# Kernel tuning notes

Hardware: AMD Instinct MI355X
Metric: run time of the kernel (lower is better)

The kernel has to match this reference:

```python
import jax, jax.numpy as jnp
import numpy as np

N, M, E, F, OUT = 20000, 2048, 320000, 512, 2
HID = F // 2
NEG_ATT = 0.2   # leaky_relu slope inside HypergraphConv attention
NEG = 0.01      # default F.leaky_relu / nn.LeakyReLU slope
EPS = 1e-5      # GraphNorm eps


def setup_inputs() -> dict:
    key = jax.random.key(0)
    ks = jax.random.split(key, 12)
    nrm = lambda k, shape, s=0.05: (jax.random.normal(k, shape, jnp.float32) * s)
    row = jax.random.randint(ks[1], (E,), 0, N)
    col = jax.random.randint(ks[2], (E,), 0, M)
    return dict(
        x=nrm(ks[0], (N, F), 1.0),
        edge_index=jnp.stack([row, col]),                 # [2, E] int32
        edge_attr=nrm(ks[3], (M, F), 1.0),
        W1=nrm(ks[4], (F, F)), att1=nrm(ks[5], (2 * F,)), b1=jnp.zeros((F,), jnp.float32),
        W2=nrm(ks[6], (F, F)), att2=nrm(ks[7], (2 * F,)), b2=jnp.zeros((F,), jnp.float32),
        gn1_w=jnp.ones((F,), jnp.float32), gn1_b=jnp.zeros((F,), jnp.float32), gn1_ms=jnp.ones((F,), jnp.float32),
        gn2_w=jnp.ones((F,), jnp.float32), gn2_b=jnp.zeros((F,), jnp.float32), gn2_ms=jnp.ones((F,), jnp.float32),
        fc1_W=nrm(ks[8], (F, HID)), fc1_b=jnp.zeros((HID,), jnp.float32),
        fc2_W=nrm(ks[9], (F, HID)), fc2_b=jnp.zeros((HID,), jnp.float32),
        cls_W=nrm(ks[10], (HID, OUT)), cls_b=jnp.zeros((OUT,), jnp.float32),
    )


def _segsum(v, idx, n):
    return jax.ops.segment_sum(v, idx, num_segments=n)


def hypergraph_conv(x, edge_attr, row, col, W, att, bias):
    """PyG HypergraphConv, heads=1, use_attention=True, attention_mode='node'."""
    xl = x @ W                          # [N, F] node features after lin
    el = edge_attr @ W                  # [M, F] hyperedge features after lin
    # attention logits per incidence: (cat[x_i, e_j] * att).sum(-1)
    pre = xl[row] @ att[:F] + el[col] @ att[F:]           # [E]
    alpha = jax.nn.leaky_relu(pre, NEG_ATT)
    # softmax grouped by hyperedge (col)
    amax = jax.ops.segment_max(alpha, col, num_segments=M)
    amax = jnp.where(jnp.isfinite(amax), amax, 0.0)
    ex = jnp.exp(alpha - amax[col])
    denom = _segsum(ex, col, M)
    alpha = ex / jnp.maximum(denom, 1e-16)[col]           # [E]
    # degree normalizations (hyperedge_weight = 1)
    ones = jnp.ones((row.shape[0],), xl.dtype)
    deg_n = _segsum(ones, row, N)
    Dinv = jnp.where(deg_n > 0, 1.0 / deg_n, 0.0)         # [N]
    deg_e = _segsum(ones, col, M)
    Binv = jnp.where(deg_e > 0, 1.0 / deg_e, 0.0)         # [M]
    # propagate 1: nodes -> hyperedges
    edge_feat = _segsum((alpha * Binv[col])[:, None] * xl[row], col, M)   # [M, F]
    # propagate 2: hyperedges -> nodes
    out = _segsum((alpha * Dinv[row])[:, None] * edge_feat[col], row, N)  # [N, F]
    return out + bias


def graph_norm(x, w, b, ms):
    # single graph (batch=None): normalize over all nodes
    mean = x.mean(axis=0)
    out = x - ms * mean
    var = (out * out).mean(axis=0)
    return out / jnp.sqrt(var + EPS) * w + b


def reference(x, edge_index, edge_attr,
              W1, att1, b1, W2, att2, b2,
              gn1_w, gn1_b, gn1_ms, gn2_w, gn2_b, gn2_ms,
              fc1_W, fc1_b, fc2_W, fc2_b, cls_W, cls_b):
    row, col = edge_index[0], edge_index[1]
    h = hypergraph_conv(x, edge_attr, row, col, W1, att1, b1)
    h = jax.nn.leaky_relu(graph_norm(h, gn1_w, gn1_b, gn1_ms), NEG)
    out = jax.nn.leaky_relu(h @ fc1_W + fc1_b, NEG)
    h = hypergraph_conv(h, edge_attr, row, col, W2, att2, b2)
    h = jax.nn.leaky_relu(graph_norm(h, gn2_w, gn2_b, gn2_ms), NEG)
    out = out + jax.nn.leaky_relu(h @ fc2_W + fc2_b, NEG)
    logits = out @ cls_W + cls_b
    return logits
```

## Files before the change

### kernel.cpp

```cpp
#include <hip/hip_runtime.h>
#include <math.h>

#define FDIM 512
#define HIDDIM 256
#define HB 128
#define SCH 1024
#define LDSK 32

typedef __bf16 bf16x8 __attribute__((ext_vector_type(8)));
typedef float floatx4 __attribute__((ext_vector_type(4)));

__device__ __forceinline__ float lrelu(float x, float s) { return x >= 0.0f ? x : s * x; }

__device__ __forceinline__ float bf2f(unsigned int u) {
  union { float f; unsigned int i; } v; v.i = u << 16; return v.f;
}
__device__ __forceinline__ unsigned short f2bf(float f) {
  union { float f; unsigned int u; } v; v.f = f;
  unsigned int x = v.u;
  return (unsigned short)((x + 0x7fffu + ((x >> 16) & 1u)) >> 16);
}

__device__ __forceinline__ void async_copy16(const unsigned short* g, unsigned short* l) {
  __builtin_amdgcn_global_load_lds((const __attribute__((address_space(1))) unsigned int*)g,
                                   (__attribute__((address_space(3))) unsigned int*)l, 16, 0, 0);
}

__device__ __forceinline__ float waveReduceSum(float v) {
#pragma unroll
  for (int o = 32; o; o >>= 1) v += __shfl_down(v, o, 64);
  return v;
}

__device__ __forceinline__ float blockReduceSum256(float v) {
  __shared__ float sm[4];
  int lane = threadIdx.x & 63, w = threadIdx.x >> 6;
  v = waveReduceSum(v);
  __syncthreads();
  if (lane == 0) sm[w] = v;
  __syncthreads();
  return sm[0] + sm[1] + sm[2] + sm[3];
}

__device__ __forceinline__ float blockReduceMax256(float v) {
  __shared__ float sm[4];
  int lane = threadIdx.x & 63, w = threadIdx.x >> 6;
#pragma unroll
  for (int o = 32; o; o >>= 1) v = fmaxf(v, __shfl_down(v, o, 64));
  __syncthreads();
  if (lane == 0) sm[w] = v;
  __syncthreads();
  return fmaxf(fmaxf(sm[0], sm[1]), fmaxf(sm[2], sm[3]));
}

__global__ __launch_bounds__(256) void k_hist2(const int* __restrict__ row, const int* __restrict__ col,
                                               int* __restrict__ cnt_r, int* __restrict__ cnt_c,
                                               int E, int nchunk) {
  __shared__ int h[2048];
  int b = blockIdx.x, t = threadIdx.x;
  for (int i = t; i < 2048; i += 256) h[i] = 0;
  __syncthreads();
  int s = b * nchunk, e = min(E, s + nchunk);
  for (int j = s + t; j < e; j += 256) {
    atomicAdd(&h[col[j]], 1);
    atomicAdd(&cnt_r[row[j]], 1);
  }
  __syncthreads();
  for (int i = t; i < 2048; i += 256) {
    int v = h[i];
    if (v) atomicAdd(&cnt_c[i], v);
  }
}

__global__ __launch_bounds__(256) void k_scan_part(const int* __restrict__ cnt, int* __restrict__ off,
                                                   int* __restrict__ btot, int n) {
  int b = blockIdx.x, t = threadIdx.x;
  int base = b * SCH + t * 4;
  int v[4];
#pragma unroll
  for (int i = 0; i < 4; ++i) v[i] = (base + i < n) ? cnt[base + i] : 0;
  int s = v[0] + v[1] + v[2] + v[3];
  int lane = t & 63, w = t >> 6;
  int x = s;
#pragma unroll
  for (int o = 1; o < 64; o <<= 1) {
    int y = __shfl_up(x, o, 64);
    if (lane >= o) x += y;
  }
  __shared__ int ws[4];
  if (lane == 63) ws[w] = x;
  __syncthreads();
  int wpre = 0;
  for (int i = 0; i < w; ++i) wpre += ws[i];
  int run = wpre + x - s;
#pragma unroll
  for (int i = 0; i < 4; ++i) {
    if (base + i < n) off[base + i] = run;
    run += v[i];
  }
  if (t == 255) btot[b] = wpre + x;
}

__global__ __launch_bounds__(256) void k_scan_mid(int* __restrict__ btot, int nb) {
  int t = threadIdx.x;
  int v = (t < nb) ? btot[t] : 0;
  int lane = t & 63, w = t >> 6;
  int x = v;
#pragma unroll
  for (int o = 1; o < 64; o <<= 1) {
    int y = __shfl_up(x, o, 64);
    if (lane >= o) x += y;
  }
  __shared__ int ws[4];
  if (lane == 63) ws[w] = x;
  __syncthreads();
  int wpre = 0;
  for (int i = 0; i < w; ++i) wpre += ws[i];
  if (t < nb) btot[t] = wpre + x - v;
  if (t == 255) btot[nb] = wpre + x;
}

__global__ __launch_bounds__(256) void k_scan_add(int* __restrict__ off, const int* __restrict__ btot,
                                                  int n, int nb) {
  int b = blockIdx.x, t = threadIdx.x;
  int base = b * SCH + t * 4;
  int add = btot[b];
#pragma unroll
  for (int i = 0; i < 4; ++i)
    if (base + i < n) off[base + i] += add;
  if (b == 0 && t == 0) off[n] = btot[nb];
}

__global__ __launch_bounds__(256) void k_scan2048(const int* __restrict__ cnt, int* __restrict__ off,
                                                  int* __restrict__ gcur) {
  int t = threadIdx.x;
  int base = t * 8;
  int v[8];
#pragma unroll
  for (int i = 0; i < 8; ++i) v[i] = cnt[base + i];
  int s = 0;
#pragma unroll
  for (int i = 0; i < 8; ++i) s += v[i];
  int lane = t & 63, w = t >> 6;
  int x = s;
#pragma unroll
  for (int o = 1; o < 64; o <<= 1) {
    int y = __shfl_up(x, o, 64);
    if (lane >= o) x += y;
  }
  __shared__ int ws[4];
  if (lane == 63) ws[w] = x;
  __syncthreads();
  int wpre = 0;
  for (int i = 0; i < w; ++i) wpre += ws[i];
  int run = wpre + x - s;
#pragma unroll
  for (int i = 0; i < 8; ++i) {
    off[base + i] = run;
    gcur[base + i] = run;
    run += v[i];
  }
  if (t == 255) off[2048] = wpre + x;
}

__global__ __launch_bounds__(256) void k_fill3(const int* __restrict__ row, const int* __restrict__ col,
                                               int* __restrict__ gcur, const int* __restrict__ off_r,
                                               int* __restrict__ cur_r, int* __restrict__ csr_c,
                                               int* __restrict__ rj, int* __restrict__ cj,
                                               int* __restrict__ pos_r, int E, int nchunk) {
  __shared__ int h[2048];
  __shared__ int lbase[2048];
  int b = blockIdx.x, t = threadIdx.x;
  for (int i = t; i < 2048; i += 256) h[i] = 0;
  __syncthreads();
  int s = b * nchunk, e = min(E, s + nchunk);
  for (int j = s + t; j < e; j += 256) atomicAdd(&h[col[j]], 1);
  __syncthreads();
  for (int i = t; i < 2048; i += 256) {
    int c = h[i];
    lbase[i] = c ? atomicAdd(&gcur[i], c) : 0;
    h[i] = 0;
  }
  __syncthreads();
  for (int j = s + t; j < e; j += 256) {
    int r = row[j], c = col[j];
    int slot_c = lbase[c] + atomicAdd(&h[c], 1);
    csr_c[slot_c] = j;
    rj[slot_c] = r;
    int slot_r = off_r[r] + atomicAdd(&cur_r[r], 1);
    cj[slot_r] = c;
    pos_r[j] = slot_r;
  }
}

__global__ __launch_bounds__(256) void k_sortseg(int* __restrict__ rj, int* __restrict__ csr_c,
                                                 const int* __restrict__ off_c) {
  int m = blockIdx.x;
  int s = off_c[m], e = off_c[m + 1];
  int n = e - s;
  if (n > 512) return;
  __shared__ int key[512];
  __shared__ int val[512];
  int t = threadIdx.x;
  for (int i = t; i < 512; i += 256) {
    if (i < n) { key[i] = rj[s + i]; val[i] = csr_c[s + i]; }
    else { key[i] = 0x7fffffff; val[i] = 0; }
  }
  __syncthreads();
  for (int k = 2; k <= 512; k <<= 1) {
    for (int j = k >> 1; j > 0; j >>= 1) {
#pragma unroll
      for (int p = 0; p < 2; ++p) {
        int i = t + p * 256;
        int ixj = i ^ j;
        if (ixj > i) {
          bool up = ((i & k) == 0);
          int a = key[i], b = key[ixj];
          if ((a > b) == up) {
            key[i] = b; key[ixj] = a;
            int va = val[i]; val[i] = val[ixj]; val[ixj] = va;
          }
        }
      }
      __syncthreads();
    }
  }
  for (int i = t; i < n; i += 256) {
    rj[s + i] = key[i];
    csr_c[s + i] = val[i];
  }
}

__global__ __launch_bounds__(256) void k_hi(const float* __restrict__ A, unsigned short* __restrict__ hi, int n4) {
  int i = blockIdx.x * 256 + threadIdx.x;
  if (i < n4) {
    float4 v = ((const float4*)A)[i];
    ushort4 h;
    h.x = f2bf(v.x); h.y = f2bf(v.y); h.z = f2bf(v.z); h.w = f2bf(v.w);
    ((ushort4*)hi)[i] = h;
  }
}

__global__ __launch_bounds__(256) void k_prep_w_hi(const float* __restrict__ W, unsigned short* __restrict__ th,
                                                   int K, int Nc) {
  int n = blockIdx.x * 16 + (threadIdx.x & 15);
  int k = blockIdx.y * 16 + (threadIdx.x >> 4);
  th[(size_t)n * K + k] = f2bf(W[(size_t)k * Nc + n]);
}

__global__ __launch_bounds__(256) void k_prep_w(const float* __restrict__ W, unsigned short* __restrict__ th,
                                                unsigned short* __restrict__ tl, int K, int Nc) {
  int n = blockIdx.x * 16 + (threadIdx.x & 15);
  int k = blockIdx.y * 16 + (threadIdx.x >> 4);
  float v = W[(size_t)k * Nc + n];
  unsigned short h = f2bf(v);
  unsigned short l = f2bf(v - bf2f(h));
  th[(size_t)n * K + k] = h;
  tl[(size_t)n * K + k] = l;
}

__global__ __launch_bounds__(256) void k_wv2(const float* __restrict__ W1, const float* __restrict__ a1,
                                             const float* __restrict__ W2, const float* __restrict__ a2,
                                             float* __restrict__ wv1, float* __restrict__ wv2) {
  int lane = threadIdx.x & 63, w = threadIdx.x >> 6;
  int k = blockIdx.x * 4 + w;
  const float* W = blockIdx.y ? W2 : W1;
  const float* a = blockIdx.y ? a2 : a1;
  float* wv = blockIdx.y ? wv2 : wv1;
  float s = 0.f;
  for (int f = lane; f < FDIM; f += 64) s = fmaf(W[(size_t)k * FDIM + f], a[f], s);
  s = waveReduceSum(s);
  if (lane == 0) wv[k] = s;
}

__global__ __launch_bounds__(256) void k_ea2(const float* __restrict__ X, const float* __restrict__ wv1,
                                             const float* __restrict__ wv2, float* __restrict__ ea1,
                                             float* __restrict__ ea2, int Mr) {
  int lane = threadIdx.x & 63, w = threadIdx.x >> 6;
  int m = blockIdx.x * 4 + w;
  if (m < Mr) {
    float s1 = 0.f, s2 = 0.f;
    for (int f = lane; f < FDIM; f += 64) {
      float v = X[(size_t)m * FDIM + f];
      s1 = fmaf(v, wv1[f], s1);
      s2 = fmaf(v, wv2[f], s2);
    }
    s1 = waveReduceSum(s1);
    s2 = waveReduceSum(s2);
    if (lane == 0) { ea1[m] = s1; ea2[m] = s2; }
  }
}

__global__ __launch_bounds__(256, 1) void gemm_conv(const unsigned short* __restrict__ Ah,
                                                    const unsigned short* __restrict__ Bth,
                                                    unsigned short* __restrict__ Cb,
                                                    const float* __restrict__ att, float* __restrict__ xa,
                                                    int Mr, int K, int Nc) {
  __shared__ unsigned short lds[2 * 128 * LDSK];
  int tid = threadIdx.x, lane = tid & 63, w = tid >> 6;
  int wr = w >> 1, wc = w & 1;
  int rowB = blockIdx.y * 128, colB = blockIdx.x * 128;

  const unsigned short* src = (w < 2) ? Ah : Bth;
  int baseRow = ((w < 2) ? rowB : colB) + 64 * (w & 1);
  int maxRow = (w < 2) ? (Mr - 1) : (Nc - 1);
  int slr = lane >> 2, slc = lane & 3;
  unsigned short* dstBase = &lds[((w >> 1) * 128 + (w & 1) * 64) * LDSK];

  size_t gro[4];
#pragma unroll
  for (int seg = 0; seg < 4; ++seg) {
    int rg = baseRow + seg * 16 + slr;
    if (rg > maxRow) rg = maxRow;
    gro[seg] = (size_t)rg * K + slc * 8;
  }

  floatx4 zero4 = {0.f, 0.f, 0.f, 0.f};
  floatx4 acc[4][4];
#pragma unroll
  for (int i = 0; i < 4; ++i)
#pragma unroll
    for (int j = 0; j < 4; ++j) acc[i][j] = zero4;

  int fr = lane & 15, fq = lane >> 4;
  int offA = (wr * 64 + fr) * LDSK + fq * 8;
  int offB = 128 * LDSK + (wc * 64 + fr) * LDSK + fq * 8;

  for (int k0 = 0; k0 < K; k0 += 32) {
#pragma unroll
    for (int seg = 0; seg < 4; ++seg) async_copy16(src + gro[seg] + k0, dstBase + seg * 16 * LDSK);
    __syncthreads();
    bf16x8 a[4], b[4];
#pragma unroll
    for (int t = 0; t < 4; ++t) {
      a[t] = *(const bf16x8*)(&lds[offA + t * 16 * LDSK]);
      b[t] = *(const bf16x8*)(&lds[offB + t * 16 * LDSK]);
    }
#pragma unroll
    for (int ti = 0; ti < 4; ++ti)
#pragma unroll
      for (int tj = 0; tj < 4; ++tj)
        acc[ti][tj] = __builtin_amdgcn_mfma_f32_16x16x32_bf16(a[ti], b[tj], acc[ti][tj], 0, 0, 0);
    __syncthreads();
  }

  int colL = colB + wc * 64 + fr;
  int rowL = rowB + wr * 64 + fq * 4;
  float attv[4];
#pragma unroll
  for (int tj = 0; tj < 4; ++tj) attv[tj] = att[colL + tj * 16];
#pragma unroll
  for (int ti = 0; ti < 4; ++ti) {
#pragma unroll
    for (int r = 0; r < 4; ++r) {
      int rr = rowL + ti * 16 + r;
      if (rr < Mr) {
        float dot = 0.f;
#pragma unroll
        for (int tj = 0; tj < 4; ++tj) {
          float v = acc[ti][tj][r];
          Cb[(size_t)rr * Nc + colL + tj * 16] = f2bf(v);
          dot = fmaf(v, attv[tj], dot);
        }
#pragma unroll
        for (int o = 1; o < 16; o <<= 1) dot += __shfl_xor(dot, o, 64);
        if ((lane & 15) == 0) atomicAdd(&xa[rr], dot);
      }
    }
  }
}

template <int EPI>
__global__ __launch_bounds__(256, 1) void gemm_fc(const unsigned short* __restrict__ Ahi,
                                                  const unsigned short* __restrict__ Bthi,
                                                  const unsigned short* __restrict__ Btlo,
                                                  float* __restrict__ Cf, const float* __restrict__ bias,
                                                  int Mr, int K, int Nc) {
  __shared__ unsigned short lds[3 * 128 * LDSK];
  int tid = threadIdx.x, lane = tid & 63, w = tid >> 6;
  int wr = w >> 1, wc = w & 1;
  int rowB = blockIdx.y * 128, colB = blockIdx.x * 128;

  const unsigned short* src;
  int baseRow, maxRow, nseg;
  unsigned short* dstBase;
  if (w < 2) { src = Ahi; baseRow = rowB + 64 * w; maxRow = Mr - 1; nseg = 4; dstBase = &lds[w * 64 * LDSK]; }
  else if (w == 2) { src = Bthi; baseRow = colB; maxRow = Nc - 1; nseg = 8; dstBase = &lds[128 * LDSK]; }
  else { src = Btlo; baseRow = colB; maxRow = Nc - 1; nseg = 8; dstBase = &lds[2 * 128 * LDSK]; }

  int slr = lane >> 2, slc = lane & 3;
  size_t gro[8];
  for (int seg = 0; seg < nseg; ++seg) {
    int rg = baseRow + seg * 16 + slr;
    if (rg > maxRow) rg = maxRow;
    gro[seg] = (size_t)rg * K + slc * 8;
  }

  floatx4 zero4 = {0.f, 0.f, 0.f, 0.f};
  floatx4 acc[4][4];
#pragma unroll
  for (int i = 0; i < 4; ++i)
#pragma unroll
    for (int j = 0; j < 4; ++j) acc[i][j] = zero4;

  int fr = lane & 15, fq = lane >> 4;
  int offA = (wr * 64 + fr) * LDSK + fq * 8;
  int offBh = 128 * LDSK + (wc * 64 + fr) * LDSK + fq * 8;

  for (int k0 = 0; k0 < K; k0 += 32) {
    for (int seg = 0; seg < nseg; ++seg) async_copy16(src + gro[seg] + k0, dstBase + seg * 16 * LDSK);
    __syncthreads();
    bf16x8 a[4], bh[4], bl[4];
#pragma unroll
    for (int t = 0; t < 4; ++t) {
      a[t] = *(const bf16x8*)(&lds[offA + t * 16 * LDSK]);
      bh[t] = *(const bf16x8*)(&lds[offBh + t * 16 * LDSK]);
      bl[t] = *(const bf16x8*)(&lds[128 * LDSK + offBh + t * 16 * LDSK]);
    }
#pragma unroll
    for (int ti = 0; ti < 4; ++ti)
#pragma unroll
      for (int tj = 0; tj < 4; ++tj) {
        acc[ti][tj] = __builtin_amdgcn_mfma_f32_16x16x32_bf16(a[ti], bh[tj], acc[ti][tj], 0, 0, 0);
        acc[ti][tj] = __builtin_amdgcn_mfma_f32_16x16x32_bf16(a[ti], bl[tj], acc[ti][tj], 0, 0, 0);
      }
    __syncthreads();
  }

  int colL = colB + wc * 64 + fr;
  int rowL = rowB + wr * 64 + fq * 4;
#pragma unroll
  for (int tj = 0; tj < 4; ++tj) {
    int c = colL + tj * 16;
    float bb = bias[c];
#pragma unroll
    for (int ti = 0; ti < 4; ++ti) {
#pragma unroll
      for (int r = 0; r < 4; ++r) {
        int rr = rowL + ti * 16 + r;
        if (rr < Mr) {
          float v = lrelu(acc[ti][tj][r] + bb, 0.01f);
          if (EPI == 1) Cf[(size_t)rr * Nc + c] = v;
          else Cf[(size_t)rr * Nc + c] += v;
        }
      }
    }
  }
}

__global__ __launch_bounds__(256) void k_attn(const float* __restrict__ xa, const float* __restrict__ ea,
                                              const int* __restrict__ rj, const int* __restrict__ csr_c,
                                              const int* __restrict__ pos_r, const int* __restrict__ off_c,
                                              float* __restrict__ aj, float* __restrict__ arj) {
  int m = blockIdx.x;
  int s = off_c[m], e_ = off_c[m + 1];
  float eam = ea[m];
  int t = threadIdx.x;
  float mx = -3.402823466e38f;
  for (int j = s + t; j < e_; j += 256) {
    float a = lrelu(xa[rj[j]] + eam, 0.2f);
    aj[j] = a;
    mx = fmaxf(mx, a);
  }
  mx = blockReduceMax256(mx);
  float sum = 0.f;
  for (int j = s + t; j < e_; j += 256) sum += expf(aj[j] - mx);
  sum = blockReduceSum256(sum);
  float inv = 1.0f / fmaxf(sum, 1e-16f);
  for (int j = s + t; j < e_; j += 256) {
    float a = expf(aj[j] - mx) * inv;
    aj[j] = a;
    arj[pos_r[csr_c[j]]] = a;
  }
}

__global__ __launch_bounds__(256) void k_prop_col(const unsigned short* __restrict__ xl,
                                                  const float* __restrict__ aj, const int* __restrict__ rj,
                                                  const int* __restrict__ off_c, unsigned short* __restrict__ ef) {
  int m = blockIdx.x;
  int s = off_c[m], e_ = off_c[m + 1];
  int cnt = e_ - s;
  __shared__ int sidx[512];
  __shared__ float swgt[512];
  __shared__ float pf[4][512];
  int t = threadIdx.x, lane = t & 63, w = t >> 6;
  float acc[8] = {0, 0, 0, 0, 0, 0, 0, 0};
  for (int base = 0; base < cnt; base += 512) {
    int n = min(512, cnt - base);
    for (int j = t; j < n; j += 256) {
      sidx[j] = rj[s + base + j];
      swgt[j] = aj[s + base + j];
    }
    __syncthreads();
    int j = w;
    for (; j + 16 <= n; j += 16) {
      int r0 = sidx[j], r1 = sidx[j + 4], r2 = sidx[j + 8], r3 = sidx[j + 12];
      float w0 = swgt[j], w1 = swgt[j + 4], w2 = swgt[j + 8], w3 = swgt[j + 12];
      bf16x8 v0 = *(const bf16x8*)(xl + (size_t)r0 * FDIM + lane * 8);
      bf16x8 v1 = *(const bf16x8*)(xl + (size_t)r1 * FDIM + lane * 8);
      bf16x8 v2 = *(const bf16x8*)(xl + (size_t)r2 * FDIM + lane * 8);
      bf16x8 v3 = *(const bf16x8*)(xl + (size_t)r3 * FDIM + lane * 8);
#pragma unroll
      for (int i = 0; i < 8; ++i) acc[i] = fmaf(w0, (float)v0[i], acc[i]);
#pragma unroll
      for (int i = 0; i < 8; ++i) acc[i] = fmaf(w1, (float)v1[i], acc[i]);
#pragma unroll
      for (int i = 0; i < 8; ++i) acc[i] = fmaf(w2, (float)v2[i], acc[i]);
#pragma unroll
      for (int i = 0; i < 8; ++i) acc[i] = fmaf(w3, (float)v3[i], acc[i]);
    }
    for (; j < n; j += 4) {
      int r = sidx[j];
      float wt = swgt[j];
      bf16x8 v = *(const bf16x8*)(xl + (size_t)r * FDIM + lane * 8);
#pragma unroll
      for (int i = 0; i < 8; ++i) acc[i] = fmaf(wt, (float)v[i], acc[i]);
    }
    __syncthreads();
  }
  float binv = cnt > 0 ? 1.0f / (float)cnt : 0.0f;
#pragma unroll
  for (int i = 0; i < 8; i += 2) *(float2*)&pf[w][lane * 8 + i] = make_float2(acc[i] * binv, acc[i + 1] * binv);
  __syncthreads();
  float2 r0 = ((const float2*)pf[0])[t], r1 = ((const float2*)pf[1])[t];
  float2 r2 = ((const float2*)pf[2])[t], r3 = ((const float2*)pf[3])[t];
  float a0 = r0.x + r1.x + r2.x + r3.x;
  float a1 = r0.y + r1.y + r2.y + r3.y;
  unsigned int o = (unsigned int)f2bf(a0) | ((unsigned int)f2bf(a1) << 16);
  ((unsigned int*)(ef + (size_t)m * FDIM))[t] = o;
}

__global__ __launch_bounds__(256) void k_prop_row(const unsigned short* __restrict__ ef,
                                                  const float* __restrict__ arj, const int* __restrict__ cj,
                                                  const int* __restrict__ off_r, const float* __restrict__ bias,
                                                  unsigned short* __restrict__ hb) {
  int nB = blockIdx.x;
  int s = off_r[nB], e_ = off_r[nB + 1];
  int cnt = e_ - s;
  __shared__ int sidx[512];
  __shared__ float swgt[512];
  __shared__ float pf[4][512];
  int t = threadIdx.x, lane = t & 63, w = t >> 6;
  float acc[8] = {0, 0, 0, 0, 0, 0, 0, 0};
  for (int base = 0; base < cnt; base += 512) {
    int n = min(512, cnt - base);
    for (int j = t; j < n; j += 256) {
      sidx[j] = cj[s + base + j];
      swgt[j] = arj[s + base + j];
    }
    __syncthreads();
    int j = w;
    for (; j + 8 <= n; j += 8) {
      int r0 = sidx[j], r1 = sidx[j + 4];
      float w0 = swgt[j], w1 = swgt[j + 4];
      bf16x8 v0 = *(const bf16x8*)(ef + (size_t)r0 * FDIM + lane * 8);
      bf16x8 v1 = *(const bf16x8*)(ef + (size_t)r1 * FDIM + lane * 8);
#pragma unroll
      for (int i = 0; i < 8; ++i) acc[i] = fmaf(w0, (float)v0[i], acc[i]);
#pragma unroll
      for (int i = 0; i < 8; ++i) acc[i] = fmaf(w1, (float)v1[i], acc[i]);
    }
    for (; j < n; j += 4) {
      int r = sidx[j];
      float wt = swgt[j];
      bf16x8 v = *(const bf16x8*)(ef + (size_t)r * FDIM + lane * 8);
#pragma unroll
      for (int i = 0; i < 8; ++i) acc[i] = fmaf(wt, (float)v[i], acc[i]);
    }
    __syncthreads();
  }
  float dinv = cnt > 0 ? 1.0f / (float)cnt : 0.0f;
#pragma unroll
  for (int i = 0; i < 8; i += 2) *(float2*)&pf[w][lane * 8 + i] = make_float2(acc[i] * dinv, acc[i + 1] * dinv);
  __syncthreads();
  float2 r0 = ((const float2*)pf[0])[t], r1 = ((const float2*)pf[1])[t];
  float2 r2 = ((const float2*)pf[2])[t], r3 = ((const float2*)pf[3])[t];
  float a0 = r0.x + r1.x + r2.x + r3.x + bias[2 * t];
  float a1 = r0.y + r1.y + r2.y + r3.y + bias[2 * t + 1];
  unsigned int o = (unsigned int)f2bf(a0) | ((unsigned int)f2bf(a1) << 16);
  ((unsigned int*)(hb + (size_t)nB * FDIM))[t] = o;
}

__global__ __launch_bounds__(256) void k_stats(const unsigned short* __restrict__ hb, float* __restrict__ gsum,
                                               float* __restrict__ gsq, int N) {
  int t = threadIdx.x;
  float s0 = 0, q0 = 0, s1 = 0, q1 = 0;
  for (int r = blockIdx.x; r < N; r += gridDim.x) {
    unsigned int u = ((const unsigned int*)(hb + (size_t)r * FDIM))[t];
    float v0 = bf2f(u & 0xffffu), v1 = bf2f(u >> 16);
    s0 += v0; q0 = fmaf(v0, v0, q0);
    s1 += v1; q1 = fmaf(v1, v1, q1);
  }
  atomicAdd(&gsum[2 * t], s0);
  atomicAdd(&gsq[2 * t], q0);
  atomicAdd(&gsum[2 * t + 1], s1);
  atomicAdd(&gsq[2 * t + 1], q1);
}

__global__ __launch_bounds__(512) void k_nparam(const float* __restrict__ gsum, const float* __restrict__ gsq,
                                                const float* __restrict__ ms, const float* __restrict__ w,
                                                float* __restrict__ msm, float* __restrict__ scl, float invn) {
  int f = threadIdx.x;
  float mean = gsum[f] * invn;
  float ex2 = gsq[f] * invn;
  float m = ms[f];
  float var = ex2 - (2.0f * m - m * m) * mean * mean;
  scl[f] = w[f] / sqrtf(var + 1e-5f);
  msm[f] = m * mean;
}

__global__ __launch_bounds__(256) void k_napply(const unsigned short* __restrict__ hb,
                                                const float* __restrict__ msm, const float* __restrict__ scl,
                                                const float* __restrict__ b, unsigned short* __restrict__ hi,
                                                int total2) {
  int i = blockIdx.x * 256 + threadIdx.x;
  if (i < total2) {
    int f2 = i & 255;
    unsigned int u = ((const unsigned int*)hb)[i];
    float v0 = bf2f(u & 0xffffu), v1 = bf2f(u >> 16);
    int f0 = 2 * f2, f1 = 2 * f2 + 1;
    v0 = lrelu((v0 - msm[f0]) * scl[f0] + b[f0], 0.01f);
    v1 = lrelu((v1 - msm[f1]) * scl[f1] + b[f1], 0.01f);
    ((unsigned int*)hi)[i] = (unsigned int)f2bf(v0) | ((unsigned int)f2bf(v1) << 16);
  }
}

__global__ __launch_bounds__(256) void k_cls(const float* __restrict__ out1, const float* __restrict__ W,
                                             const float* __restrict__ b, float* __restrict__ logits, int N) {
  __shared__ float Ws[512];
  int t = threadIdx.x;
  Ws[t] = W[t];
  Ws[256 + t] = W[256 + t];
  __syncthreads();
  int lane = t & 63, w = t >> 6;
  int r = blockIdx.x * 4 + w;
  if (r < N) {
    float a0 = 0.f, a1 = 0.f;
    for (int k = lane; k < 256; k += 64) {
      float v = out1[(size_t)r * 256 + k];
      a0 = fmaf(v, Ws[2 * k], a0);
      a1 = fmaf(v, Ws[2 * k + 1], a1);
    }
#pragma unroll
    for (int o = 32; o; o >>= 1) {
      a0 += __shfl_down(a0, o, 64);
      a1 += __shfl_down(a1, o, 64);
    }
    if (lane == 0) {
      logits[(size_t)r * 2] = a0 + b[0];
      logits[(size_t)r * 2 + 1] = a1 + b[1];
    }
  }
}

extern "C" void kernel_launch(void* const* d_in, const int* in_sizes, int n_in,
                              void* d_out, int out_size, void* d_ws, size_t ws_size,
                              hipStream_t stream) {
  const float* x      = (const float*)d_in[0];
  const int*   eidx   = (const int*)d_in[1];
  const float* eattr  = (const float*)d_in[2];
  const float* W1     = (const float*)d_in[3];
  const float* att1   = (const float*)d_in[4];
  const float* b1     = (const float*)d_in[5];
  const float* W2     = (const float*)d_in[6];
  const float* att2   = (const float*)d_in[7];
  const float* b2     = (const float*)d_in[8];
  const float* gn1_w  = (const float*)d_in[9];
  const float* gn1_b  = (const float*)d_in[10];
  const float* gn1_ms = (const float*)d_in[11];
  const float* gn2_w  = (const float*)d_in[12];
  const float* gn2_b  = (const float*)d_in[13];
  const float* gn2_ms = (const float*)d_in[14];
  const float* fc1_W  = (const float*)d_in[15];
  const float* fc1_b  = (const float*)d_in[16];
  const float* fc2_W  = (const float*)d_in[17];
  const float* fc2_b  = (const float*)d_in[18];
  const float* cls_W  = (const float*)d_in[19];
  const float* cls_b  = (const float*)d_in[20];
  float* logits = (float*)d_out;

  const int N = in_sizes[0] / FDIM;
  const int E = in_sizes[1] / 2;
  const int M = in_sizes[2] / FDIM;
  const int* row = eidx;
  const int* col = eidx + E;
  const size_t NS = (size_t)N * FDIM;
  const size_t MS = (size_t)M * FDIM;

  char* base = (char*)d_ws;
  auto alloc = [&](size_t bytes) { char* r = base; base += (bytes + 255) & ~(size_t)255; return r; };

  unsigned short* xhi = (unsigned short*)alloc(NS * 2);
  unsigned short* xl  = (unsigned short*)alloc(NS * 2);
  unsigned short* hb  = (unsigned short*)alloc(NS * 2);
  unsigned short* ef  = (unsigned short*)alloc(MS * 2);
  float* out1 = (float*)alloc((size_t)N * HIDDIM * 4);
  unsigned short* w1th = (unsigned short*)alloc(FDIM * FDIM * 2);
  unsigned short* w2th = (unsigned short*)alloc(FDIM * FDIM * 2);
  unsigned short* f1th = (unsigned short*)alloc(FDIM * HIDDIM * 2);
  unsigned short* f1tl = (unsigned short*)alloc(FDIM * HIDDIM * 2);
  unsigned short* f2th = (unsigned short*)alloc(FDIM * HIDDIM * 2);
  unsigned short* f2tl = (unsigned short*)alloc(FDIM * HIDDIM * 2);
  float* wv1 = (float*)alloc(FDIM * 4);
  float* wv2 = (float*)alloc(FDIM * 4);
  float* xa = (float*)alloc((size_t)N * 4);
  float* ea1 = (float*)alloc((size_t)M * 4);
  float* ea2 = (float*)alloc((size_t)M * 4);
  float* aj  = (float*)alloc((size_t)E * 4);
  float* arj = (float*)alloc((size_t)E * 4);
  float* gsum = (float*)alloc(FDIM * 4);
  float* gsq  = (float*)alloc(FDIM * 4);
  float* msm  = (float*)alloc(FDIM * 4);
  float* scl  = (float*)alloc(FDIM * 4);
  int* cnt_r = (int*)alloc((size_t)(2 * N + M) * 4);
  int* cur_r = cnt_r + N;
  int* cnt_c = cur_r + N;
  int* off_r = (int*)alloc((size_t)(N + 1) * 4);
  int* off_c = (int*)alloc((size_t)(M + 1) * 4);
  int* gcur  = (int*)alloc((size_t)M * 4);
  int* csr_c = (int*)alloc((size_t)E * 4);
  int* rj    = (int*)alloc((size_t)E * 4);
  int* cj    = (int*)alloc((size_t)E * 4);
  int* pos_r = (int*)alloc((size_t)E * 4);
  int* btot  = (int*)alloc(512 * 4);

  hipMemsetAsync(cnt_r, 0, sizeof(int) * (size_t)(2 * N + M), stream);

  int nchunk = (E + HB - 1) / HB;
  int nbR = (N + SCH - 1) / SCH;
  k_hist2<<<HB, 256, 0, stream>>>(row, col, cnt_r, cnt_c, E, nchunk);
  k_scan_part<<<nbR, 256, 0, stream>>>(cnt_r, off_r, btot, N);
  k_scan_mid<<<1, 256, 0, stream>>>(btot, nbR);
  k_scan_add<<<nbR, 256, 0, stream>>>(off_r, btot, N, nbR);
  k_scan2048<<<1, 256, 0, stream>>>(cnt_c, off_c, gcur);
  k_fill3<<<HB, 256, 0, stream>>>(row, col, gcur, off_r, cur_r, csr_c, rj, cj, pos_r, E, nchunk);
  k_sortseg<<<M, 256, 0, stream>>>(rj, csr_c, off_c);

  k_hi<<<(int)((NS / 4 + 255) / 256), 256, 0, stream>>>(x, xhi, (int)(NS / 4));
  k_prep_w_hi<<<dim3(FDIM / 16, FDIM / 16), 256, 0, stream>>>(W1, w1th, FDIM, FDIM);
  k_prep_w_hi<<<dim3(FDIM / 16, FDIM / 16), 256, 0, stream>>>(W2, w2th, FDIM, FDIM);
  k_prep_w<<<dim3(HIDDIM / 16, FDIM / 16), 256, 0, stream>>>(fc1_W, f1th, f1tl, FDIM, HIDDIM);
  k_prep_w<<<dim3(HIDDIM / 16, FDIM / 16), 256, 0, stream>>>(fc2_W, f2th, f2tl, FDIM, HIDDIM);
  k_wv2<<<dim3(FDIM / 4, 2), 256, 0, stream>>>(W1, att1 + FDIM, W2, att2 + FDIM, wv1, wv2);
  k_ea2<<<(M + 3) / 4, 256, 0, stream>>>(eattr, wv1, wv2, ea1, ea2, M);

  int gN128 = (N + 127) / 128;
  int napply_grid = (int)((NS / 2 + 255) / 256);

  hipMemsetAsync(xa, 0, (size_t)N * 4, stream);
  gemm_conv<<<dim3(FDIM / 128, gN128), 256, 0, stream>>>(xhi, w1th, xl, att1, xa, N, FDIM, FDIM);
  k_attn<<<M, 256, 0, stream>>>(xa, ea1, rj, csr_c, pos_r, off_c, aj, arj);
  k_prop_col<<<M, 256, 0, stream>>>(xl, aj, rj, off_c, ef);
  k_prop_row<<<N, 256, 0, stream>>>(ef, arj, cj, off_r, b1, hb);
  hipMemsetAsync(gsum, 0, sizeof(float) * 2 * FDIM, stream);
  k_stats<<<256, 256, 0, stream>>>(hb, gsum, gsq, N);
  k_nparam<<<1, 512, 0, stream>>>(gsum, gsq, gn1_ms, gn1_w, msm, scl, 1.0f / (float)N);
  k_napply<<<napply_grid, 256, 0, stream>>>(hb, msm, scl, gn1_b, xhi, (int)(NS / 2));
  gemm_fc<1><<<dim3(HIDDIM / 128, gN128), 256, 0, stream>>>(xhi, f1th, f1tl, out1, fc1_b, N, FDIM, HIDDIM);

  hipMemsetAsync(xa, 0, (size_t)N * 4, stream);
  gemm_conv<<<dim3(FDIM / 128, gN128), 256, 0, stream>>>(xhi, w2th, xl, att2, xa, N, FDIM, FDIM);
  k_attn<<<M, 256, 0, stream>>>(xa, ea2, rj, csr_c, pos_r, off_c, aj, arj);
  k_prop_col<<<M, 256, 0, stream>>>(xl, aj, rj, off_c, ef);
  k_prop_row<<<N, 256, 0, stream>>>(ef, arj, cj, off_r, b2, hb);
  hipMemsetAsync(gsum, 0, sizeof(float) * 2 * FDIM, stream);
  k_stats<<<256, 256, 0, stream>>>(hb, gsum, gsq, N);
  k_nparam<<<1, 512, 0, stream>>>(gsum, gsq, gn2_ms, gn2_w, msm, scl, 1.0f / (float)N);
  k_napply<<<napply_grid, 256, 0, stream>>>(hb, msm, scl, gn2_b, xhi, (int)(NS / 2));
  gemm_fc<2><<<dim3(HIDDIM / 128, gN128), 256, 0, stream>>>(xhi, f2th, f2tl, out1, fc2_b, N, FDIM, HIDDIM);

  k_cls<<<(N + 3) / 4, 256, 0, stream>>>(out1, cls_W, cls_b, logits, N);
}
```

Measured before the change: 601.8 us.

## Fuse attention softmax into column propagation and cut small launches and memsets

Attention softmax is folded into the column-propagation kernel, which recomputes logits from xa instead of storing and rereading a per-incidence buffer. The per-segment bitonic sort is dropped, and the column scan is merged into the mid-scan kernel. Weight preparation is batched into two launches, the norm-parameter kernel is folded into napply, and all zeroing becomes one memset. The cost is recomputing exp/lrelu three times per incidence; dropping the sort changes the order of segment sums, which may change rounding and access locality.

```diff
diff --git a/kernel.cpp b/kernel.cpp
--- a/kernel.cpp
+++ b/kernel.cpp
@@ -101,23 +101,52 @@
   if (t == 255) btot[b] = wpre + x;
 }
 
-__global__ __launch_bounds__(256) void k_scan_mid(int* __restrict__ btot, int nb) {
-  int t = threadIdx.x;
-  int v = (t < nb) ? btot[t] : 0;
-  int lane = t & 63, w = t >> 6;
-  int x = v;
-#pragma unroll
-  for (int o = 1; o < 64; o <<= 1) {
-    int y = __shfl_up(x, o, 64);
-    if (lane >= o) x += y;
-  }
+__global__ __launch_bounds__(256) void k_scan_midcol(int* __restrict__ btot, int nb,
+                                                     const int* __restrict__ cnt_c, int* __restrict__ off_c,
+                                                     int* __restrict__ gcur) {
+  int t = threadIdx.x, lane = t & 63, w = t >> 6;
   __shared__ int ws[4];
-  if (lane == 63) ws[w] = x;
-  __syncthreads();
-  int wpre = 0;
-  for (int i = 0; i < w; ++i) wpre += ws[i];
-  if (t < nb) btot[t] = wpre + x - v;
-  if (t == 255) btot[nb] = wpre + x;
+  if (blockIdx.x == 0) {
+    int v = (t < nb) ? btot[t] : 0;
+    int x = v;
+#pragma unroll
+    for (int o = 1; o < 64; o <<= 1) {
+      int y = __shfl_up(x, o, 64);
+      if (lane >= o) x += y;
+    }
+    if (lane == 63) ws[w] = x;
+    __syncthreads();
+    int wpre = 0;
+    for (int i = 0; i < w; ++i) wpre += ws[i];
+    if (t < nb) btot[t] = wpre + x - v;
+    if (t == 255) btot[nb] = wpre + x;
+  } else {
+    int base = t * 8;
+    int v[8];
+#pragma unroll
+    for (int i = 0; i < 8; ++i) v[i] = cnt_c[base + i];
+    int s = 0;
+#pragma unroll
+    for (int i = 0; i < 8; ++i) s += v[i];
+    int x = s;
+#pragma unroll
+    for (int o = 1; o < 64; o <<= 1) {
+      int y = __shfl_up(x, o, 64);
+      if (lane >= o) x += y;
+    }
+    if (lane == 63) ws[w] = x;
+    __syncthreads();
+    int wpre = 0;
+    for (int i = 0; i < w; ++i) wpre += ws[i];
+    int run = wpre + x - s;
+#pragma unroll
+    for (int i = 0; i < 8; ++i) {
+      off_c[base + i] = run;
+      gcur[base + i] = run;
+      run += v[i];
+    }
+    if (t == 255) off_c[2048] = wpre + x;
+  }
 }
 
 __global__ __launch_bounds__(256) void k_scan_add(int* __restrict__ off, const int* __restrict__ btot,
@@ -129,38 +158,6 @@
   for (int i = 0; i < 4; ++i)
     if (base + i < n) off[base + i] += add;
   if (b == 0 && t == 0) off[n] = btot[nb];
-}
-
-__global__ __launch_bounds__(256) void k_scan2048(const int* __restrict__ cnt, int* __restrict__ off,
-                                                  int* __restrict__ gcur) {
-  int t = threadIdx.x;
-  int base = t * 8;
-  int v[8];
-#pragma unroll
-  for (int i = 0; i < 8; ++i) v[i] = cnt[base + i];
-  int s = 0;
-#pragma unroll
-  for (int i = 0; i < 8; ++i) s += v[i];
-  int lane = t & 63, w = t >> 6;
-  int x = s;
-#pragma unroll
-  for (int o = 1; o < 64; o <<= 1) {
-    int y = __shfl_up(x, o, 64);
-    if (lane >= o) x += y;
-  }
-  __shared__ int ws[4];
-  if (lane == 63) ws[w] = x;
-  __syncthreads();
-  int wpre = 0;
-  for (int i = 0; i < w; ++i) wpre += ws[i];
-  int run = wpre + x - s;
-#pragma unroll
-  for (int i = 0; i < 8; ++i) {
-    off[base + i] = run;
-    gcur[base + i] = run;
-    run += v[i];
-  }
-  if (t == 255) off[2048] = wpre + x;
 }
 
 __global__ __launch_bounds__(256) void k_fill3(const int* __restrict__ row, const int* __restrict__ col,
@@ -193,44 +190,6 @@
   }
 }
 
-__global__ __launch_bounds__(256) void k_sortseg(int* __restrict__ rj, int* __restrict__ csr_c,
-                                                 const int* __restrict__ off_c) {
-  int m = blockIdx.x;
-  int s = off_c[m], e = off_c[m + 1];
-  int n = e - s;
-  if (n > 512) return;
-  __shared__ int key[512];
-  __shared__ int val[512];
-  int t = threadIdx.x;
-  for (int i = t; i < 512; i += 256) {
-    if (i < n) { key[i] = rj[s + i]; val[i] = csr_c[s + i]; }
-    else { key[i] = 0x7fffffff; val[i] = 0; }
-  }
-  __syncthreads();
-  for (int k = 2; k <= 512; k <<= 1) {
-    for (int j = k >> 1; j > 0; j >>= 1) {
-#pragma unroll
-      for (int p = 0; p < 2; ++p) {
-        int i = t + p * 256;
-        int ixj = i ^ j;
-        if (ixj > i) {
-          bool up = ((i & k) == 0);
-          int a = key[i], b = key[ixj];
-          if ((a > b) == up) {
-            key[i] = b; key[ixj] = a;
-            int va = val[i]; val[i] = val[ixj]; val[ixj] = va;
-          }
-        }
-      }
-      __syncthreads();
-    }
-  }
-  for (int i = t; i < n; i += 256) {
-    rj[s + i] = key[i];
-    csr_c[s + i] = val[i];
-  }
-}
-
 __global__ __launch_bounds__(256) void k_hi(const float* __restrict__ A, unsigned short* __restrict__ hi, int n4) {
   int i = blockIdx.x * 256 + threadIdx.x;
   if (i < n4) {
@@ -241,15 +200,23 @@
   }
 }
 
-__global__ __launch_bounds__(256) void k_prep_w_hi(const float* __restrict__ W, unsigned short* __restrict__ th,
-                                                   int K, int Nc) {
+__global__ __launch_bounds__(256) void k_prep_w_hi2(const float* __restrict__ W1, unsigned short* __restrict__ t1,
+                                                    const float* __restrict__ W2, unsigned short* __restrict__ t2,
+                                                    int K, int Nc) {
+  const float* W = blockIdx.z ? W2 : W1;
+  unsigned short* th = blockIdx.z ? t2 : t1;
   int n = blockIdx.x * 16 + (threadIdx.x & 15);
   int k = blockIdx.y * 16 + (threadIdx.x >> 4);
   th[(size_t)n * K + k] = f2bf(W[(size_t)k * Nc + n]);
 }
 
-__global__ __launch_bounds__(256) void k_prep_w(const float* __restrict__ W, unsigned short* __restrict__ th,
-                                                unsigned short* __restrict__ tl, int K, int Nc) {
+__global__ __launch_bounds__(256) void k_prep_w2(const float* __restrict__ Wa, unsigned short* __restrict__ tha,
+                                                 unsigned short* __restrict__ tla, const float* __restrict__ Wb,
+                                                 unsigned short* __restrict__ thb, unsigned short* __restrict__ tlb,
+                                                 int K, int Nc) {
+  const float* W = blockIdx.z ? Wb : Wa;
+  unsigned short* th = blockIdx.z ? thb : tha;
+  unsigned short* tl = blockIdx.z ? tlb : tla;
   int n = blockIdx.x * 16 + (threadIdx.x & 15);
   int k = blockIdx.y * 16 + (threadIdx.x >> 4);
   float v = W[(size_t)k * Nc + n];
@@ -448,48 +415,38 @@
   }
 }
 
-__global__ __launch_bounds__(256) void k_attn(const float* __restrict__ xa, const float* __restrict__ ea,
-                                              const int* __restrict__ rj, const int* __restrict__ csr_c,
-                                              const int* __restrict__ pos_r, const int* __restrict__ off_c,
-                                              float* __restrict__ aj, float* __restrict__ arj) {
-  int m = blockIdx.x;
-  int s = off_c[m], e_ = off_c[m + 1];
-  float eam = ea[m];
-  int t = threadIdx.x;
-  float mx = -3.402823466e38f;
-  for (int j = s + t; j < e_; j += 256) {
-    float a = lrelu(xa[rj[j]] + eam, 0.2f);
-    aj[j] = a;
-    mx = fmaxf(mx, a);
-  }
-  mx = blockReduceMax256(mx);
-  float sum = 0.f;
-  for (int j = s + t; j < e_; j += 256) sum += expf(aj[j] - mx);
-  sum = blockReduceSum256(sum);
-  float inv = 1.0f / fmaxf(sum, 1e-16f);
-  for (int j = s + t; j < e_; j += 256) {
-    float a = expf(aj[j] - mx) * inv;
-    aj[j] = a;
-    arj[pos_r[csr_c[j]]] = a;
-  }
-}
-
-__global__ __launch_bounds__(256) void k_prop_col(const unsigned short* __restrict__ xl,
-                                                  const float* __restrict__ aj, const int* __restrict__ rj,
-                                                  const int* __restrict__ off_c, unsigned short* __restrict__ ef) {
+__global__ __launch_bounds__(256) void k_prop_col_f(const unsigned short* __restrict__ xl,
+                                                    const float* __restrict__ xa, const float* __restrict__ ea,
+                                                    const int* __restrict__ rj, const int* __restrict__ csr_c,
+                                                    const int* __restrict__ pos_r, const int* __restrict__ off_c,
+                                                    float* __restrict__ arj, unsigned short* __restrict__ ef) {
   int m = blockIdx.x;
   int s = off_c[m], e_ = off_c[m + 1];
   int cnt = e_ - s;
+  float eam = ea[m];
+  int t = threadIdx.x, lane = t & 63, w = t >> 6;
+
+  float mx = -3.402823466e38f;
+  for (int j = s + t; j < e_; j += 256) mx = fmaxf(mx, lrelu(xa[rj[j]] + eam, 0.2f));
+  mx = blockReduceMax256(mx);
+  float sum = 0.f;
+  for (int j = s + t; j < e_; j += 256) sum += expf(lrelu(xa[rj[j]] + eam, 0.2f) - mx);
+  sum = blockReduceSum256(sum);
+  float inv = 1.0f / fmaxf(sum, 1e-16f);
+
   __shared__ int sidx[512];
   __shared__ float swgt[512];
   __shared__ float pf[4][512];
-  int t = threadIdx.x, lane = t & 63, w = t >> 6;
   float acc[8] = {0, 0, 0, 0, 0, 0, 0, 0};
   for (int base = 0; base < cnt; base += 512) {
     int n = min(512, cnt - base);
     for (int j = t; j < n; j += 256) {
-      sidx[j] = rj[s + base + j];
-      swgt[j] = aj[s + base + j];
+      int g = s + base + j;
+      int r = rj[g];
+      float a = expf(lrelu(xa[r] + eam, 0.2f) - mx) * inv;
+      sidx[j] = r;
+      swgt[j] = a;
+      arj[pos_r[csr_c[g]]] = a;
     }
     __syncthreads();
     int j = w;
@@ -597,30 +554,25 @@
   atomicAdd(&gsq[2 * t + 1], q1);
 }
 
-__global__ __launch_bounds__(512) void k_nparam(const float* __restrict__ gsum, const float* __restrict__ gsq,
-                                                const float* __restrict__ ms, const float* __restrict__ w,
-                                                float* __restrict__ msm, float* __restrict__ scl, float invn) {
-  int f = threadIdx.x;
-  float mean = gsum[f] * invn;
-  float ex2 = gsq[f] * invn;
-  float m = ms[f];
-  float var = ex2 - (2.0f * m - m * m) * mean * mean;
-  scl[f] = w[f] / sqrtf(var + 1e-5f);
-  msm[f] = m * mean;
-}
-
 __global__ __launch_bounds__(256) void k_napply(const unsigned short* __restrict__ hb,
-                                                const float* __restrict__ msm, const float* __restrict__ scl,
+                                                const float* __restrict__ gsum, const float* __restrict__ gsq,
+                                                const float* __restrict__ ms, const float* __restrict__ wg,
                                                 const float* __restrict__ b, unsigned short* __restrict__ hi,
-                                                int total2) {
+                                                float invn, int total2) {
   int i = blockIdx.x * 256 + threadIdx.x;
   if (i < total2) {
     int f2 = i & 255;
+    int f0 = 2 * f2, f1 = 2 * f2 + 1;
+    float mean0 = gsum[f0] * invn, mean1 = gsum[f1] * invn;
+    float m0 = ms[f0], m1 = ms[f1];
+    float var0 = gsq[f0] * invn - (2.0f * m0 - m0 * m0) * mean0 * mean0;
+    float var1 = gsq[f1] * invn - (2.0f * m1 - m1 * m1) * mean1 * mean1;
+    float scl0 = wg[f0] * __frsqrt_rn(var0 + 1e-5f);
+    float scl1 = wg[f1] * __frsqrt_rn(var1 + 1e-5f);
     unsigned int u = ((const unsigned int*)hb)[i];
     float v0 = bf2f(u & 0xffffu), v1 = bf2f(u >> 16);
-    int f0 = 2 * f2, f1 = 2 * f2 + 1;
-    v0 = lrelu((v0 - msm[f0]) * scl[f0] + b[f0], 0.01f);
-    v1 = lrelu((v1 - msm[f1]) * scl[f1] + b[f1], 0.01f);
+    v0 = lrelu((v0 - m0 * mean0) * scl0 + b[f0], 0.01f);
+    v1 = lrelu((v1 - m1 * mean1) * scl1 + b[f1], 0.01f);
     ((unsigned int*)hi)[i] = (unsigned int)f2bf(v0) | ((unsigned int)f2bf(v1) << 16);
   }
 }
@@ -703,18 +655,9 @@
   unsigned short* f2tl = (unsigned short*)alloc(FDIM * HIDDIM * 2);
   float* wv1 = (float*)alloc(FDIM * 4);
   float* wv2 = (float*)alloc(FDIM * 4);
-  float* xa = (float*)alloc((size_t)N * 4);
   float* ea1 = (float*)alloc((size_t)M * 4);
   float* ea2 = (float*)alloc((size_t)M * 4);
-  float* aj  = (float*)alloc((size_t)E * 4);
   float* arj = (float*)alloc((size_t)E * 4);
-  float* gsum = (float*)alloc(FDIM * 4);
-  float* gsq  = (float*)alloc(FDIM * 4);
-  float* msm  = (float*)alloc(FDIM * 4);
-  float* scl  = (float*)alloc(FDIM * 4);
-  int* cnt_r = (int*)alloc((size_t)(2 * N + M) * 4);
-  int* cur_r = cnt_r + N;
-  int* cnt_c = cur_r + N;
   int* off_r = (int*)alloc((size_t)(N + 1) * 4);
   int* off_c = (int*)alloc((size_t)(M + 1) * 4);
   int* gcur  = (int*)alloc((size_t)M * 4);
@@ -724,49 +667,49 @@
   int* pos_r = (int*)alloc((size_t)E * 4);
   int* btot  = (int*)alloc(512 * 4);
 
-  hipMemsetAsync(cnt_r, 0, sizeof(int) * (size_t)(2 * N + M), stream);
+  char* zstart = base;
+  int* cnt_r = (int*)alloc((size_t)(2 * N + M) * 4);
+  int* cur_r = cnt_r + N;
+  int* cnt_c = cur_r + N;
+  float* xa1 = (float*)alloc((size_t)N * 4);
+  float* xa2 = (float*)alloc((size_t)N * 4);
+  float* gsum1 = (float*)alloc(FDIM * 4);
+  float* gsq1  = (float*)alloc(FDIM * 4);
+  float* gsum2 = (float*)alloc(FDIM * 4);
+  float* gsq2  = (float*)alloc(FDIM * 4);
+  size_t zlen = (size_t)(base - zstart);
+  hipMemsetAsync(zstart, 0, zlen, stream);
 
   int nchunk = (E + HB - 1) / HB;
   int nbR = (N + SCH - 1) / SCH;
   k_hist2<<<HB, 256, 0, stream>>>(row, col, cnt_r, cnt_c, E, nchunk);
   k_scan_part<<<nbR, 256, 0, stream>>>(cnt_r, off_r, btot, N);
-  k_scan_mid<<<1, 256, 0, stream>>>(btot, nbR);
+  k_scan_midcol<<<2, 256, 0, stream>>>(btot, nbR, cnt_c, off_c, gcur);
   k_scan_add<<<nbR, 256, 0, stream>>>(off_r, btot, N, nbR);
-  k_scan2048<<<1, 256, 0, stream>>>(cnt_c, off_c, gcur);
   k_fill3<<<HB, 256, 0, stream>>>(row, col, gcur, off_r, cur_r, csr_c, rj, cj, pos_r, E, nchunk);
-  k_sortseg<<<M, 256, 0, stream>>>(rj, csr_c, off_c);
 
   k_hi<<<(int)((NS / 4 + 255) / 256), 256, 0, stream>>>(x, xhi, (int)(NS / 4));
-  k_prep_w_hi<<<dim3(FDIM / 16, FDIM / 16), 256, 0, stream>>>(W1, w1th, FDIM, FDIM);
-  k_prep_w_hi<<<dim3(FDIM / 16, FDIM / 16), 256, 0, stream>>>(W2, w2th, FDIM, FDIM);
-  k_prep_w<<<dim3(HIDDIM / 16, FDIM / 16), 256, 0, stream>>>(fc1_W, f1th, f1tl, FDIM, HIDDIM);
-  k_prep_w<<<dim3(HIDDIM / 16, FDIM / 16), 256, 0, stream>>>(fc2_W, f2th, f2tl, FDIM, HIDDIM);
+  k_prep_w_hi2<<<dim3(FDIM / 16, FDIM / 16, 2), 256, 0, stream>>>(W1, w1th, W2, w2th, FDIM, FDIM);
+  k_prep_w2<<<dim3(HIDDIM / 16, FDIM / 16, 2), 256, 0, stream>>>(fc1_W, f1th, f1tl, fc2_W, f2th, f2tl, FDIM, HIDDIM);
   k_wv2<<<dim3(FDIM / 4, 2), 256, 0, stream>>>(W1, att1 + FDIM, W2, att2 + FDIM, wv1, wv2);
   k_ea2<<<(M + 3) / 4, 256, 0, stream>>>(eattr, wv1, wv2, ea1, ea2, M);
 
   int gN128 = (N + 127) / 128;
   int napply_grid = (int)((NS / 2 + 255) / 256);
-
-  hipMemsetAsync(xa, 0, (size_t)N * 4, stream);
-  gemm_conv<<<dim3(FDIM / 128, gN128), 256, 0, stream>>>(xhi, w1th, xl, att1, xa, N, FDIM, FDIM);
-  k_attn<<<M, 256, 0, stream>>>(xa, ea1, rj, csr_c, pos_r, off_c, aj, arj);
-  k_prop_col<<<M, 256, 0, stream>>>(xl, aj, rj, off_c, ef);
+  float invn = 1.0f / (float)N;
+
+  gemm_conv<<<dim3(FDIM / 128, gN128), 256, 0, stream>>>(xhi, w1th, xl, att1, xa1, N, FDIM, FDIM);
+  k_prop_col_f<<<M, 256, 0, stream>>>(xl, xa1, ea1, rj, csr_c, pos_r, off_c, arj, ef);
   k_prop_row<<<N, 256, 0, stream>>>(ef, arj, cj, off_r, b1, hb);
-  hipMemsetAsync(gsum, 0, sizeof(float) * 2 * FDIM, stream);
-  k_stats<<<256, 256, 0, stream>>>(hb, gsum, gsq, N);
-  k_nparam<<<1, 512, 0, stream>>>(gsum, gsq, gn1_ms, gn1_w, msm, scl, 1.0f / (float)N);
-  k_napply<<<napply_grid, 256, 0, stream>>>(hb, msm, scl, gn1_b, xhi, (int)(NS / 2));
+  k_stats<<<256, 256, 0, stream>>>(hb, gsum1, gsq1, N);
+  k_napply<<<napply_grid, 256, 0, stream>>>(hb, gsum1, gsq1, gn1_ms, gn1_w, gn1_b, xhi, invn, (int)(NS / 2));
   gemm_fc<1><<<dim3(HIDDIM / 128, gN128), 256, 0, stream>>>(xhi, f1th, f1tl, out1, fc1_b, N, FDIM, HIDDIM);
 
-  hipMemsetAsync(xa, 0, (size_t)N * 4, stream);
-  gemm_conv<<<dim3(FDIM / 128, gN128), 256, 0, stream>>>(xhi, w2th, xl, att2, xa, N, FDIM, FDIM);
-  k_attn<<<M, 256, 0, stream>>>(xa, ea2, rj, csr_c, pos_r, off_c, aj, arj);
-  k_prop_col<<<M, 256, 0, stream>>>(xl, aj, rj, off_c, ef);
+  gemm_conv<<<dim3(FDIM / 128, gN128), 256, 0, stream>>>(xhi, w2th, xl, att2, xa2, N, FDIM, FDIM);
+  k_prop_col_f<<<M, 256, 0, stream>>>(xl, xa2, ea2, rj, csr_c, pos_r, off_c, arj, ef);
   k_prop_row<<<N, 256, 0, stream>>>(ef, arj, cj, off_r, b2, hb);
-  hipMemsetAsync(gsum, 0, sizeof(float) * 2 * FDIM, stream);
-  k_stats<<<256, 256, 0, stream>>>(hb, gsum, gsq, N);
-  k_nparam<<<1, 512, 0, stream>>>(gsum, gsq, gn2_ms, gn2_w, msm, scl, 1.0f / (float)N);
-  k_napply<<<napply_grid, 256, 0, stream>>>(hb, msm, scl, gn2_b, xhi, (int)(NS / 2));
+  k_stats<<<256, 256, 0, stream>>>(hb, gsum2, gsq2, N);
+  k_napply<<<napply_grid, 256, 0, stream>>>(hb, gsum2, gsq2, gn2_ms, gn2_w, gn2_b, xhi, invn, (int)(NS / 2));
   gemm_fc<2><<<dim3(HIDDIM / 128, gN128), 256, 0, stream>>>(xhi, f2th, f2tl, out1, fc2_b, N, FDIM, HIDDIM);
 
   k_cls<<<(N + 3) / 4, 256, 0, stream>>>(out1, cls_W, cls_b, logits, N);
```

After: 579.5 us. 1.04x faster.
